# Kernel tuning notes

Hardware: AMD Instinct MI355X
Metric: run time of the kernel (lower is better)

Reference implementation:

```python
import jax, jax.numpy as jnp
import numpy as np
from jax import lax

SCORE_THRESHOLD = 0.5
IOU_THRESHOLD = 0.5
N_ANCHORS = 8400


def setup_inputs() -> dict:
    key = jax.random.key(0)
    yolo_raw_output = jax.random.uniform(key, (1, 5, N_ANCHORS), dtype=jnp.float32)
    return {"yolo_raw_output": yolo_raw_output}


def _pairwise_iou(boxes):
    # boxes: [N, 4] in xyxy
    x1, y1, x2, y2 = boxes[:, 0], boxes[:, 1], boxes[:, 2], boxes[:, 3]
    area = (x2 - x1) * (y2 - y1)                       # [N]
    lt_x = jnp.maximum(x1[:, None], x1[None, :])       # [N, N]
    lt_y = jnp.maximum(y1[:, None], y1[None, :])
    rb_x = jnp.minimum(x2[:, None], x2[None, :])
    rb_y = jnp.minimum(y2[:, None], y2[None, :])
    inter = jnp.clip(rb_x - lt_x, 0.0) * jnp.clip(rb_y - lt_y, 0.0)
    union = area[:, None] + area[None, :] - inter
    return inter / union


def reference(yolo_raw_output):
    # [1, 5, N] -> [N, 5]
    out = jnp.transpose(yolo_raw_output, (0, 2, 1))[0]
    scores = out[:, 4]
    valid = scores > SCORE_THRESHOLD            # score filter (mask, fixed shape)

    # cxcywh -> xyxy
    cx, cy, w, h = out[:, 0], out[:, 1], out[:, 2], out[:, 3]
    xyxy = jnp.stack([cx - w * 0.5, cy - h * 0.5, cx + w * 0.5, cy + h * 0.5], axis=1)

    # sort by score descending (invalid pushed to the end)
    masked_scores = jnp.where(valid, scores, -jnp.inf)
    order = jnp.argsort(-masked_scores)
    boxes_s = xyxy[order]                       # [N, 4]
    scores_s = jnp.where(valid, scores, 0.0)[order]
    valid_s = valid[order]

    # NMS: pairwise IoU + sequential suppression over sorted boxes
    iou = _pairwise_iou(lax.stop_gradient(boxes_s))
    suppress = iou > IOU_THRESHOLD              # [N, N] bool
    idx = jnp.arange(boxes_s.shape[0])

    def body(i, keep):
        # box i suppresses later boxes only if it itself is kept
        sup = suppress[i] & keep[i] & (idx > i)
        return keep & ~sup

    keep = lax.fori_loop(0, boxes_s.shape[0], body, valid_s)

    boxes_and_scores = jnp.concatenate([boxes_s, scores_s[:, None]], axis=1)  # [N, 5]
    # fixed-shape analogue of boxes_and_scores[selected_indices]:
    # suppressed / below-threshold rows are zeroed, kept rows are score-sorted.
    return jnp.where(keep[:, None], boxes_and_scores, 0.0)
```

## Files before the change

kernel.cpp:

```cpp
#include <hip/hip_runtime.h>
#include <cstdint>

#define N_ANCH 8400
#define WMAX   132
#define NB     (WMAX * 64)
#define NT     512
#define CSLOT  32

__device__ __forceinline__ uint64_t readlane64(uint64_t v, int lane) {
  unsigned lo = (unsigned)__builtin_amdgcn_readlane((int)(unsigned)(v & 0xffffffffull), lane);
  unsigned hi = (unsigned)__builtin_amdgcn_readlane((int)(unsigned)(v >> 32), lane);
  return ((uint64_t)hi << 32) | lo;
}
__device__ __forceinline__ uint64_t firstlane64(uint64_t v) {
  unsigned lo = (unsigned)__builtin_amdgcn_readfirstlane((int)(unsigned)(v & 0xffffffffull));
  unsigned hi = (unsigned)__builtin_amdgcn_readfirstlane((int)(unsigned)(v >> 32));
  return ((uint64_t)hi << 32) | lo;
}
__device__ __forceinline__ uint64_t shflxor64(uint64_t v, int m) {
  int lo = __shfl_xor((int)(unsigned)(v & 0xffffffffull), m, 64);
  int hi = __shfl_xor((int)(unsigned)(v >> 32), m, 64);
  return ((uint64_t)(unsigned)hi << 32) | (unsigned)lo;
}

__global__ __launch_bounds__(256) void k_rank(const float* __restrict__ in,
                                              float* __restrict__ scores_s,
                                              float4* __restrict__ boxes_s,
                                              unsigned* __restrict__ nvp) {
  __shared__ alignas(16) float sc[N_ANCH];
  __shared__ int part[256];
  const int tid = threadIdx.x;
  const float* srow = in + 4 * N_ANCH;
  for (int j = tid; j < N_ANCH; j += 256) sc[j] = srow[j];
  __syncthreads();
  const int il = tid & 63, q = tid >> 6;
  const int i = blockIdx.x * 64 + il;
  const float si = (i < N_ANCH) ? sc[i] : 0.0f;
  const bool valid = si > 0.5f;
  const float key = valid ? si : -INFINITY;
  int cnt = 0;
  const float4* sc4 = (const float4*)sc;
  const int jb = q * (N_ANCH / 4);
  for (int jj = 0; jj < (N_ANCH / 16); ++jj) {
    float4 v = sc4[q * (N_ANCH / 16) + jj];
    int j0 = jb + jj * 4;
    float k0 = (v.x > 0.5f) ? v.x : -INFINITY;
    float k1 = (v.y > 0.5f) ? v.y : -INFINITY;
    float k2 = (v.z > 0.5f) ? v.z : -INFINITY;
    float k3 = (v.w > 0.5f) ? v.w : -INFINITY;
    cnt += (k0 > key) || (k0 == key && (j0 + 0) < i);
    cnt += (k1 > key) || (k1 == key && (j0 + 1) < i);
    cnt += (k2 > key) || (k2 == key && (j0 + 2) < i);
    cnt += (k3 > key) || (k3 == key && (j0 + 3) < i);
  }
  part[tid] = cnt;
  __syncthreads();
  if (q == 0 && i < N_ANCH) {
    int r = part[il] + part[64 + il] + part[128 + il] + part[192 + il];
    float cx = in[0 * N_ANCH + i], cy = in[1 * N_ANCH + i];
    float w  = in[2 * N_ANCH + i], h  = in[3 * N_ANCH + i];
    float x1 = cx - w * 0.5f, y1 = cy - h * 0.5f;
    float x2 = cx + w * 0.5f, y2 = cy + h * 0.5f;
    boxes_s[r] = make_float4(x1, y1, x2, y2);
    scores_s[r] = valid ? si : 0.0f;
    if (valid) atomicAdd(nvp, 1u);
  }
}

__global__ __launch_bounds__(256) void k_sup(const float4* __restrict__ boxes_s,
                                             const unsigned* __restrict__ nvp,
                                             unsigned long long* __restrict__ sup,
                                             unsigned long long* __restrict__ diag) {
  const int nv = (int)*nvp;
  const int W = (nv + 63) >> 6;
  const int Wp = (W + 1) & ~1;
  const int w = blockIdx.x;
  if (w >= W) return;
  if (w + 1 < (int)(blockIdx.y * 256) >> 6) return;
  __shared__ float bx1[64], by1[64], bx2[64], by2[64], bar[64];
  const int tid = threadIdx.x;
  if (tid < 64) {
    int j = w * 64 + tid;
    float4 b = (j < N_ANCH) ? boxes_s[j] : make_float4(0.f, 0.f, 0.f, 0.f);
    bx1[tid] = b.x; by1[tid] = b.y; bx2[tid] = b.z; by2[tid] = b.w;
    bar[tid] = (b.z - b.x) * (b.w - b.y);
  }
  __syncthreads();
  const int i = blockIdx.y * 256 + tid;
  if (i >= nv) return;
  if (w < (i >> 6)) return;
  float4 bi = boxes_s[i];
  float ai = (bi.z - bi.x) * (bi.w - bi.y);
  const int jmax = nv - w * 64;
  uint64_t bits = 0;
  #pragma unroll 8
  for (int l = 0; l < 64; ++l) {
    float lx = fmaxf(bi.x, bx1[l]);
    float ly = fmaxf(bi.y, by1[l]);
    float rx = fminf(bi.z, bx2[l]);
    float ry = fminf(bi.w, by2[l]);
    float dx = fmaxf(rx - lx, 0.0f);
    float dy = fmaxf(ry - ly, 0.0f);
    float inter = dx * dy;
    asm volatile("" : "+v"(inter));
    float uni = (ai + bar[l]) - inter;
    float iou = inter / uni;
    bits |= ((uint64_t)((l < jmax) && (iou > 0.5f))) << l;
  }
  sup[(size_t)i * Wp + w] = bits;
  if (w == (i >> 6)) diag[i] = bits;
}

__global__ __launch_bounds__(NT) void k_scan(const float* __restrict__ scores_s,
                                             const float4* __restrict__ boxes_s,
                                             const unsigned long long* __restrict__ sup_,
                                             const unsigned long long* __restrict__ diag_g,
                                             const unsigned* __restrict__ nvp,
                                             float* __restrict__ out) {
  __shared__ uint64_t keep_s[WMAX];
  const uint64_t* sup = (const uint64_t*)sup_;
  const uint64_t* diag64 = (const uint64_t*)diag_g;
  const int tid = threadIdx.x;
  const int lane = tid & 63;
  const int wave = tid >> 6;
  const int nv = (int)*nvp;
  const int W  = (nv + 63) >> 6;
  const int Wp = (W + 1) & ~1;

  for (int idx = tid; idx < WMAX; idx += NT) {
    uint64_t v = 0; int base = idx * 64;
    if (base < nv) { int rem = nv - base; v = (rem >= 64) ? ~0ull : ((1ull << rem) - 1ull); }
    keep_s[idx] = v;
  }
  __syncthreads();

  if (wave == 0 && W > 0) {
    uint64_t pre[CSLOT];
    uint64_t bkw = firstlane64(keep_s[0]);
    uint64_t ovw = 0;
    uint64_t dw  = diag64[lane];

    {
      uint64_t remc = bkw;
      const int wd = 1 + lane;
      #pragma unroll
      for (int s = 0; s < CSLOT; ++s) {
        int r = remc ? (int)__builtin_ctzll(remc) : 0;
        bool valid = (remc != 0);
        remc &= remc - 1;
        pre[s] = (valid && wd < W) ? sup[(size_t)r * Wp + wd] : 0ull;
      }
      ovw = remc;
    }

    for (int k = 0; k < W; ++k) {
      uint64_t bk = bkw;
      {
        uint64_t cand = bk;
        while (cand) {
          int r = (int)__builtin_ctzll(cand);
          uint64_t sr = readlane64(dw, r);
          uint64_t m = sr & ~((2ull << r) - 1ull);
          cand &= ~(1ull << r);
          cand &= ~m;
          bk   &= ~m;
        }
      }
      if (lane == 0) keep_s[k] = bk;
      if (k + 1 < W) dw = diag64[(size_t)(k + 1) * 64 + lane];

      const int wd = k + 1 + lane;
      uint64_t acc = 0;
      {
        uint64_t remc = bkw;
        #pragma unroll
        for (int s = 0; s < CSLOT; ++s) {
          int r = remc ? (int)__builtin_ctzll(remc) : 0;
          uint64_t mk = (uint64_t)0 - (uint64_t)((remc != 0) && ((bk >> r) & 1ull));
          remc &= remc - 1;
          acc |= pre[s] & mk;
        }
      }
      {
        uint64_t remo = ovw & bk;
        const size_t rowbase = (size_t)k * 64;
        while (remo) {
          int r0 = (int)__builtin_ctzll(remo); remo &= remo - 1;
          uint64_t m1 = (uint64_t)0 - (uint64_t)(remo != 0);
          int r1 = remo ? (int)__builtin_ctzll(remo) : r0; remo &= remo - 1;
          uint64_t m2 = (uint64_t)0 - (uint64_t)(remo != 0);
          int r2 = remo ? (int)__builtin_ctzll(remo) : r0; remo &= remo - 1;
          uint64_t m3 = (uint64_t)0 - (uint64_t)(remo != 0);
          int r3 = remo ? (int)__builtin_ctzll(remo) : r0; remo &= remo - 1;
          uint64_t m4 = (uint64_t)0 - (uint64_t)(remo != 0);
          int r4 = remo ? (int)__builtin_ctzll(remo) : r0; remo &= remo - 1;
          uint64_t m5 = (uint64_t)0 - (uint64_t)(remo != 0);
          int r5 = remo ? (int)__builtin_ctzll(remo) : r0; remo &= remo - 1;
          uint64_t m6 = (uint64_t)0 - (uint64_t)(remo != 0);
          int r6 = remo ? (int)__builtin_ctzll(remo) : r0; remo &= remo - 1;
          uint64_t m7 = (uint64_t)0 - (uint64_t)(remo != 0);
          int r7 = remo ? (int)__builtin_ctzll(remo) : r0; remo &= remo - 1;
          if (wd < W) {
            uint64_t v0 = sup[(rowbase + r0) * Wp + wd];
            uint64_t v1 = sup[(rowbase + r1) * Wp + wd];
            uint64_t v2 = sup[(rowbase + r2) * Wp + wd];
            uint64_t v3 = sup[(rowbase + r3) * Wp + wd];
            uint64_t v4 = sup[(rowbase + r4) * Wp + wd];
            uint64_t v5 = sup[(rowbase + r5) * Wp + wd];
            uint64_t v6 = sup[(rowbase + r6) * Wp + wd];
            uint64_t v7 = sup[(rowbase + r7) * Wp + wd];
            acc |= v0 | (v1 & m1) | (v2 & m2) | (v3 & m3)
                      | (v4 & m4) | (v5 & m5) | (v6 & m6) | (v7 & m7);
          }
        }
      }
      if (wd < W) keep_s[wd] &= ~acc;

      for (int wd2 = k + 65; wd2 < W; ++wd2) {
        uint64_t v = 0;
        if ((bk >> lane) & 1ull) v = sup[((size_t)k * 64 + lane) * Wp + wd2];
        v |= shflxor64(v, 1);  v |= shflxor64(v, 2);  v |= shflxor64(v, 4);
        v |= shflxor64(v, 8);  v |= shflxor64(v, 16); v |= shflxor64(v, 32);
        if (lane == 0) keep_s[wd2] &= ~v;
      }

      if (k + 1 < W) {
        bkw = firstlane64(keep_s[k + 1]);
        uint64_t remc = bkw;
        const int wdn = k + 2 + lane;
        const size_t rb = (size_t)(k + 1) * 64;
        #pragma unroll
        for (int s = 0; s < CSLOT; ++s) {
          int r = remc ? (int)__builtin_ctzll(remc) : 0;
          bool valid = (remc != 0);
          remc &= remc - 1;
          pre[s] = (valid && wdn < W) ? sup[(rb + r) * Wp + wdn] : 0ull;
        }
        ovw = remc;
      }
    }
  }
  __syncthreads();

  for (int r = tid; r < N_ANCH; r += NT) {
    bool kept = (r < nv) && ((keep_s[r >> 6] >> (r & 63)) & 1ull);
    float4 b = kept ? boxes_s[r] : make_float4(0.f, 0.f, 0.f, 0.f);
    float s = kept ? scores_s[r] : 0.0f;
    out[r * 5 + 0] = b.x;
    out[r * 5 + 1] = b.y;
    out[r * 5 + 2] = b.z;
    out[r * 5 + 3] = b.w;
    out[r * 5 + 4] = s;
  }
}

extern "C" void kernel_launch(void* const* d_in, const int* in_sizes, int n_in,
                              void* d_out, int out_size, void* d_ws, size_t ws_size,
                              hipStream_t stream) {
  const float* in = (const float*)d_in[0];
  float* out = (float*)d_out;
  uint8_t* ws = (uint8_t*)d_ws;
  unsigned* nvp = (unsigned*)ws;
  float* scores_s = (float*)(ws + 64);
  float4* boxes_s = (float4*)(ws + 64 + 33600);
  unsigned long long* diag = (unsigned long long*)(ws + 64 + 33600 + (size_t)NB * 16);
  unsigned long long* sup  = (unsigned long long*)(ws + 64 + 33600 + (size_t)NB * 24);

  (void)hipMemsetAsync(ws, 0, 64, stream);
  k_rank<<<dim3(WMAX), dim3(256), 0, stream>>>(in, scores_s, boxes_s, nvp);
  k_sup<<<dim3(WMAX, (N_ANCH + 255) / 256), dim3(256), 0, stream>>>(boxes_s, nvp, sup, diag);
  k_scan<<<dim3(1), dim3(NT), 0, stream>>>(scores_s, boxes_s, sup, diag, nvp, out);
}
```

Measured before the change: 284.9 us.

## Double-buffer suppression-row prefetch two blocks ahead in NMS scan

The serial scan wave now holds two prefetch buffers and issues the suppression-mask loads for block k+1 before processing block k. It works from a keep word that may be stale, but that word is a superset of the final one, and the fresh keep mask still filters the results. This aims to hide global-memory latency on the serial critical path. In exchange it may load rows for boxes that later get suppressed. The block size drops to 256 threads with launch_bounds(NT,1), and the per-buffer prefetch slots go from 32 to 24 to limit register pressure.

```diff
diff --git a/kernel.cpp b/kernel.cpp
--- a/kernel.cpp
+++ b/kernel.cpp
@@ -4,8 +4,8 @@
 #define N_ANCH 8400
 #define WMAX   132
 #define NB     (WMAX * 64)
-#define NT     512
-#define CSLOT  32
+#define NT     256
+#define CSLOT  24
 
 __device__ __forceinline__ uint64_t readlane64(uint64_t v, int lane) {
   unsigned lo = (unsigned)__builtin_amdgcn_readlane((int)(unsigned)(v & 0xffffffffull), lane);
@@ -111,12 +111,12 @@
   if (w == (i >> 6)) diag[i] = bits;
 }
 
-__global__ __launch_bounds__(NT) void k_scan(const float* __restrict__ scores_s,
-                                             const float4* __restrict__ boxes_s,
-                                             const unsigned long long* __restrict__ sup_,
-                                             const unsigned long long* __restrict__ diag_g,
-                                             const unsigned* __restrict__ nvp,
-                                             float* __restrict__ out) {
+__global__ __launch_bounds__(NT, 1) void k_scan(const float* __restrict__ scores_s,
+                                                const float4* __restrict__ boxes_s,
+                                                const unsigned long long* __restrict__ sup_,
+                                                const unsigned long long* __restrict__ diag_g,
+                                                const unsigned* __restrict__ nvp,
+                                                float* __restrict__ out) {
   __shared__ uint64_t keep_s[WMAX];
   const uint64_t* sup = (const uint64_t*)sup_;
   const uint64_t* diag64 = (const uint64_t*)diag_g;
@@ -135,109 +135,105 @@
   __syncthreads();
 
   if (wave == 0 && W > 0) {
-    uint64_t pre[CSLOT];
-    uint64_t bkw = firstlane64(keep_s[0]);
-    uint64_t ovw = 0;
-    uint64_t dw  = diag64[lane];
-
-    {
-      uint64_t remc = bkw;
-      const int wd = 1 + lane;
+    uint64_t preA[CSLOT], preB[CSLOT];
+    uint64_t dwA = 0, dwB = 0;
+
+    auto issueFor = [&](int kk, uint64_t (&pre)[CSLOT], uint64_t& dwn) -> uint64_t {
+      if (kk >= W) {
+        #pragma unroll
+        for (int s = 0; s < CSLOT; ++s) pre[s] = 0;
+        return 0;
+      }
+      uint64_t cw = firstlane64(keep_s[kk]);
+      dwn = diag64[(size_t)kk * 64 + lane];
+      const int wdn = kk + 1 + lane;
+      const bool inW = (wdn < W);
+      const int wdc = inW ? wdn : 0;
+      uint64_t remc = cw;
       #pragma unroll
       for (int s = 0; s < CSLOT; ++s) {
         int r = remc ? (int)__builtin_ctzll(remc) : 0;
-        bool valid = (remc != 0);
+        bool v = (remc != 0);
         remc &= remc - 1;
-        pre[s] = (valid && wd < W) ? sup[(size_t)r * Wp + wd] : 0ull;
-      }
-      ovw = remc;
-    }
-
-    for (int k = 0; k < W; ++k) {
-      uint64_t bk = bkw;
-      {
-        uint64_t cand = bk;
-        while (cand) {
-          int r = (int)__builtin_ctzll(cand);
-          uint64_t sr = readlane64(dw, r);
-          uint64_t m = sr & ~((2ull << r) - 1ull);
-          cand &= ~(1ull << r);
-          cand &= ~m;
-          bk   &= ~m;
-        }
+        const uint64_t* base = sup + ((size_t)kk * 64 + r) * Wp;
+        uint64_t val = v ? base[wdc] : 0ull;
+        pre[s] = (v && inW) ? val : 0ull;
+      }
+      return cw;
+    };
+
+    auto useStep = [&](int k, uint64_t (&pre)[CSLOT], uint64_t dwv, uint64_t cw) {
+      uint64_t kw = firstlane64(keep_s[k]);
+      uint64_t bk = kw, cand = kw;
+      while (cand) {
+        int r = (int)__builtin_ctzll(cand);
+        uint64_t sr = readlane64(dwv, r);
+        uint64_t m = sr & ~((2ull << r) - 1ull);
+        cand &= ~(1ull << r);
+        cand &= ~m;
+        bk   &= ~m;
       }
       if (lane == 0) keep_s[k] = bk;
-      if (k + 1 < W) dw = diag64[(size_t)(k + 1) * 64 + lane];
 
       const int wd = k + 1 + lane;
       uint64_t acc = 0;
-      {
-        uint64_t remc = bkw;
-        #pragma unroll
-        for (int s = 0; s < CSLOT; ++s) {
-          int r = remc ? (int)__builtin_ctzll(remc) : 0;
-          uint64_t mk = (uint64_t)0 - (uint64_t)((remc != 0) && ((bk >> r) & 1ull));
-          remc &= remc - 1;
-          acc |= pre[s] & mk;
-        }
-      }
-      {
-        uint64_t remo = ovw & bk;
-        const size_t rowbase = (size_t)k * 64;
-        while (remo) {
-          int r0 = (int)__builtin_ctzll(remo); remo &= remo - 1;
-          uint64_t m1 = (uint64_t)0 - (uint64_t)(remo != 0);
-          int r1 = remo ? (int)__builtin_ctzll(remo) : r0; remo &= remo - 1;
-          uint64_t m2 = (uint64_t)0 - (uint64_t)(remo != 0);
-          int r2 = remo ? (int)__builtin_ctzll(remo) : r0; remo &= remo - 1;
-          uint64_t m3 = (uint64_t)0 - (uint64_t)(remo != 0);
-          int r3 = remo ? (int)__builtin_ctzll(remo) : r0; remo &= remo - 1;
-          uint64_t m4 = (uint64_t)0 - (uint64_t)(remo != 0);
-          int r4 = remo ? (int)__builtin_ctzll(remo) : r0; remo &= remo - 1;
-          uint64_t m5 = (uint64_t)0 - (uint64_t)(remo != 0);
-          int r5 = remo ? (int)__builtin_ctzll(remo) : r0; remo &= remo - 1;
-          uint64_t m6 = (uint64_t)0 - (uint64_t)(remo != 0);
-          int r6 = remo ? (int)__builtin_ctzll(remo) : r0; remo &= remo - 1;
-          uint64_t m7 = (uint64_t)0 - (uint64_t)(remo != 0);
-          int r7 = remo ? (int)__builtin_ctzll(remo) : r0; remo &= remo - 1;
-          if (wd < W) {
-            uint64_t v0 = sup[(rowbase + r0) * Wp + wd];
-            uint64_t v1 = sup[(rowbase + r1) * Wp + wd];
-            uint64_t v2 = sup[(rowbase + r2) * Wp + wd];
-            uint64_t v3 = sup[(rowbase + r3) * Wp + wd];
-            uint64_t v4 = sup[(rowbase + r4) * Wp + wd];
-            uint64_t v5 = sup[(rowbase + r5) * Wp + wd];
-            uint64_t v6 = sup[(rowbase + r6) * Wp + wd];
-            uint64_t v7 = sup[(rowbase + r7) * Wp + wd];
-            acc |= v0 | (v1 & m1) | (v2 & m2) | (v3 & m3)
-                      | (v4 & m4) | (v5 & m5) | (v6 & m6) | (v7 & m7);
-          }
+      uint64_t remc = cw;
+      #pragma unroll
+      for (int s = 0; s < CSLOT; ++s) {
+        int r = remc ? (int)__builtin_ctzll(remc) : 0;
+        uint64_t mk = (uint64_t)0 - (uint64_t)((remc != 0) && ((bk >> r) & 1ull));
+        remc &= remc - 1;
+        acc |= pre[s] & mk;
+      }
+      uint64_t remo = remc & bk;
+      const size_t rowbase = (size_t)k * 64;
+      while (remo) {
+        int r0 = (int)__builtin_ctzll(remo); remo &= remo - 1;
+        uint64_t m1 = (uint64_t)0 - (uint64_t)(remo != 0);
+        int r1 = remo ? (int)__builtin_ctzll(remo) : r0; remo &= remo - 1;
+        uint64_t m2 = (uint64_t)0 - (uint64_t)(remo != 0);
+        int r2 = remo ? (int)__builtin_ctzll(remo) : r0; remo &= remo - 1;
+        uint64_t m3 = (uint64_t)0 - (uint64_t)(remo != 0);
+        int r3 = remo ? (int)__builtin_ctzll(remo) : r0; remo &= remo - 1;
+        uint64_t m4 = (uint64_t)0 - (uint64_t)(remo != 0);
+        int r4 = remo ? (int)__builtin_ctzll(remo) : r0; remo &= remo - 1;
+        uint64_t m5 = (uint64_t)0 - (uint64_t)(remo != 0);
+        int r5 = remo ? (int)__builtin_ctzll(remo) : r0; remo &= remo - 1;
+        uint64_t m6 = (uint64_t)0 - (uint64_t)(remo != 0);
+        int r6 = remo ? (int)__builtin_ctzll(remo) : r0; remo &= remo - 1;
+        uint64_t m7 = (uint64_t)0 - (uint64_t)(remo != 0);
+        int r7 = remo ? (int)__builtin_ctzll(remo) : r0; remo &= remo - 1;
+        if (wd < W) {
+          uint64_t v0 = sup[(rowbase + r0) * Wp + wd];
+          uint64_t v1 = sup[(rowbase + r1) * Wp + wd];
+          uint64_t v2 = sup[(rowbase + r2) * Wp + wd];
+          uint64_t v3 = sup[(rowbase + r3) * Wp + wd];
+          uint64_t v4 = sup[(rowbase + r4) * Wp + wd];
+          uint64_t v5 = sup[(rowbase + r5) * Wp + wd];
+          uint64_t v6 = sup[(rowbase + r6) * Wp + wd];
+          uint64_t v7 = sup[(rowbase + r7) * Wp + wd];
+          acc |= v0 | (v1 & m1) | (v2 & m2) | (v3 & m3)
+                    | (v4 & m4) | (v5 & m5) | (v6 & m6) | (v7 & m7);
         }
       }
       if (wd < W) keep_s[wd] &= ~acc;
 
       for (int wd2 = k + 65; wd2 < W; ++wd2) {
         uint64_t v = 0;
-        if ((bk >> lane) & 1ull) v = sup[((size_t)k * 64 + lane) * Wp + wd2];
+        if ((bk >> lane) & 1ull) v = sup[(rowbase + lane) * Wp + wd2];
         v |= shflxor64(v, 1);  v |= shflxor64(v, 2);  v |= shflxor64(v, 4);
         v |= shflxor64(v, 8);  v |= shflxor64(v, 16); v |= shflxor64(v, 32);
         if (lane == 0) keep_s[wd2] &= ~v;
       }
-
-      if (k + 1 < W) {
-        bkw = firstlane64(keep_s[k + 1]);
-        uint64_t remc = bkw;
-        const int wdn = k + 2 + lane;
-        const size_t rb = (size_t)(k + 1) * 64;
-        #pragma unroll
-        for (int s = 0; s < CSLOT; ++s) {
-          int r = remc ? (int)__builtin_ctzll(remc) : 0;
-          bool valid = (remc != 0);
-          remc &= remc - 1;
-          pre[s] = (valid && wdn < W) ? sup[(rb + r) * Wp + wdn] : 0ull;
-        }
-        ovw = remc;
-      }
+    };
+
+    uint64_t cwA = issueFor(0, preA, dwA);
+    uint64_t cwB;
+    for (int k = 0; k < W; k += 2) {
+      cwB = issueFor(k + 1, preB, dwB);
+      useStep(k, preA, dwA, cwA);
+      cwA = issueFor(k + 2, preA, dwA);
+      if (k + 1 < W) useStep(k + 1, preB, dwB, cwB);
     }
   }
   __syncthreads();
```

Result: slower. 511.5 us (+79.5%).
